# Optimization experiments

Measured on AMD Instinct MI355X. Metric: run time of the kernel, lower is better.

Reference implementation:

```python
import jax, jax.numpy as jnp
import numpy as np
from functools import partial

STRIDES = (8, 16, 32)
SIZES = ((80, 80), (40, 40), (20, 20))
NUM_CLASSES = 80
NMS_THR = 0.65
SCORE_THR = 0.01
MAX_DET = 100  # fixed-size NMS output (padded; validity = scores > 0)


def setup_inputs() -> dict:
    key = jax.random.key(0)
    ks = jax.random.split(key, 9)
    B = 32
    out = {}
    for i, (h, w) in enumerate(SIZES):
        out[f"cls{i}"] = jax.random.normal(ks[3 * i], (B, NUM_CLASSES, h, w), jnp.float32)
        out[f"reg{i}"] = jax.random.normal(ks[3 * i + 1], (B, 4, h, w), jnp.float32)
        out[f"obj{i}"] = jax.random.normal(ks[3 * i + 2], (B, 1, h, w), jnp.float32)
    return out


def _grid_points():
    # MlvlPointGenerator.grid_priors(with_stride=True), offset=0: (x, y, stride, stride)
    pts = []
    for (h, w), s in zip(SIZES, STRIDES):
        xs = jnp.arange(w, dtype=jnp.float32) * s
        ys = jnp.arange(h, dtype=jnp.float32) * s
        xx, yy = jnp.meshgrid(xs, ys)  # [h, w], x varies fastest -> matches NHWC flatten
        st = jnp.full((h * w,), float(s), jnp.float32)
        pts.append(jnp.stack([xx.ravel(), yy.ravel(), st, st], axis=-1))
    return jnp.concatenate(pts, axis=0)  # [A, 4]


def _flatten(t, c):
    # [N, C, H, W] -> [N, H*W, C]  (permute(0,2,3,1).reshape)
    return t.transpose(0, 2, 3, 1).reshape(t.shape[0], -1, c)


def _decode(points, reg):
    # YOLOXBBoxDecoder: center = pred_xy * stride + point, wh = exp(pred_wh) * stride
    stride = points[:, 2:]                       # [A, 2]
    xys = reg[..., :2] * stride + points[:, :2]  # [B, A, 2]
    whs = jnp.exp(reg[..., 2:]) * stride         # [B, A, 2]
    return jnp.concatenate([xys - whs * 0.5, xys + whs * 0.5], axis=-1)  # x1y1x2y2


def _iou_one_vs_all(b, boxes):
    # b: [4], boxes: [A, 4]
    tl = jnp.maximum(b[:2], boxes[:, :2])
    br = jnp.minimum(b[2:], boxes[:, 2:])
    wh = jnp.clip(br - tl, 0.0)
    inter = wh[:, 0] * wh[:, 1]
    a1 = (b[2] - b[0]) * (b[3] - b[1])
    a2 = (boxes[:, 2] - boxes[:, 0]) * (boxes[:, 3] - boxes[:, 1])
    return inter / (a1 + a2 - inter + 1e-6)


def _nms_image(boxes, cls_scores, objectness):
    # boxes [A,4], cls_scores [A,C] (post-sigmoid), objectness [A] (post-sigmoid)
    max_scores = jnp.max(cls_scores, axis=1)
    labels = jnp.argmax(cls_scores, axis=1)
    scores = max_scores * objectness
    live = jnp.where(scores >= SCORE_THR, scores, -jnp.inf)  # score_thr filter

    # batched_nms: offset boxes per class so boxes of different labels never overlap
    offset = jax.lax.stop_gradient(jnp.max(jnp.abs(boxes)) + 1.0)
    boxes_off = jax.lax.stop_gradient(boxes) + labels.astype(boxes.dtype)[:, None] * offset

    def body(i, state):
        live, keep, kscores = state
        best = jnp.argmax(live)
        kscores = kscores.at[i].set(live[best])
        keep = keep.at[i].set(best)
        iou = _iou_one_vs_all(boxes_off[best], boxes_off)
        live = jnp.where(iou > NMS_THR, -jnp.inf, live)
        live = live.at[best].set(-jnp.inf)
        return live, keep, kscores

    keep0 = jnp.zeros((MAX_DET,), jnp.int32)
    ks0 = jnp.full((MAX_DET,), -jnp.inf, boxes.dtype)
    _, keep, kscores = jax.lax.fori_loop(0, MAX_DET, body, (live, keep0, ks0))

    valid = kscores > -jnp.inf
    out_boxes = jnp.where(valid[:, None], boxes[keep], 0.0)
    out_scores = jnp.where(valid, scores[keep], 0.0)
    out_labels = jnp.where(valid, labels[keep], -1)
    return out_boxes, out_scores, out_labels, valid


def _forward(cls0, cls1, cls2, reg0, reg1, reg2, obj0, obj1, obj2):
    B = cls0.shape[0]
    flat_cls = jax.nn.sigmoid(jnp.concatenate([_flatten(c, NUM_CLASSES) for c in (cls0, cls1, cls2)], axis=1))
    flat_reg = jnp.concatenate([_flatten(r, 4) for r in (reg0, reg1, reg2)], axis=1)
    flat_obj = jax.nn.sigmoid(jnp.concatenate([_flatten(o, 1) for o in (obj0, obj1, obj2)], axis=1))[..., 0]
    points = _grid_points()
    boxes = _decode(points, flat_reg)  # [B, A, 4]
    return jax.vmap(_nms_image)(boxes, flat_cls, flat_obj)


@jax.jit
def reference(cls0, cls1, cls2, reg0, reg1, reg2, obj0, obj1, obj2):
    return _forward(cls0, cls1, cls2, reg0, reg1, reg2, obj0, obj1, obj2)
```

## Files before the change

kernel.cpp:

```cpp
#include <hip/hip_runtime.h>
#include <cmath>

typedef unsigned int uint;
typedef unsigned long long ull;

#define BATCH 32
#define NA 8400
#define NC 80
#define MAXDET 100
#define NMSTHR 0.65f
#define SCTHR 0.01f

#define NT 1024
#define NW (NT / 64)
#define EPT 9
#define NBINS 4096
#define CAP 512

#define DGROUPS 132

__device__ __forceinline__ float stable_sigmoid(float x) {
    if (x >= 0.f) return 1.f / (1.f + expf(-x));
    float e = expf(x);
    return e / (1.f + e);
}

template<int HW, int W, int S>
__device__ __forceinline__ void decode_blk(
    const float* __restrict__ cls, const float* __restrict__ reg,
    const float* __restrict__ obj, int b, int p0, int w, int lane, int ag0,
    float (*s_m)[64], int (*s_c)[64],
    float4* __restrict__ wboxes, int* __restrict__ wlabels, uint* __restrict__ wkeys)
{
    int p = p0 + lane;
    bool valid = (p < HW);
    int pc = valid ? p : (HW - 1);

    const float* cbase = cls + (size_t)b * NC * HW + (size_t)(w * 20) * HW + pc;
    float v[20];
    #pragma unroll
    for (int i = 0; i < 20; ++i) v[i] = cbase[(size_t)i * HW];
    float m = v[0]; int c = 0;
    #pragma unroll
    for (int i = 1; i < 20; ++i)
        if (v[i] > m) { m = v[i]; c = i; }

    s_m[w][lane] = m;
    s_c[w][lane] = c + w * 20;
    __syncthreads();

    if (w == 0) {
        float mm = s_m[0][lane]; int cc = s_c[0][lane];
        #pragma unroll
        for (int ww = 1; ww < 4; ++ww) {
            float om = s_m[ww][lane]; int oc = s_c[ww][lane];
            if (om > mm) { mm = om; cc = oc; }
        }
        const float* rb = reg + (size_t)b * 4 * HW + pc;
        float r0 = rb[0];
        float r1 = rb[HW];
        float r2 = rb[2 * (size_t)HW];
        float r3 = rb[3 * (size_t)HW];
        float ov = obj[(size_t)b * HW + pc];

        int y = pc / W;
        int x = pc - y * W;
        float sc = stable_sigmoid(mm) * stable_sigmoid(ov);
        float cx = r0 * (float)S + (float)x * (float)S;
        float cy = r1 * (float)S + (float)y * (float)S;
        float bw = expf(r2) * (float)S;
        float bh = expf(r3) * (float)S;

        if (valid) {
            int ag = ag0 + lane;
            wboxes[ag]  = make_float4(cx - bw * 0.5f, cy - bh * 0.5f,
                                      cx + bw * 0.5f, cy + bh * 0.5f);
            wlabels[ag] = cc;
            wkeys[ag]   = (sc >= SCTHR) ? ~__float_as_uint(sc) : 0xFFFFFFFFu;
        }
    }
}

__global__ __launch_bounds__(256) void decode_kernel(
    const float* __restrict__ cls0, const float* __restrict__ reg0, const float* __restrict__ obj0,
    const float* __restrict__ cls1, const float* __restrict__ reg1, const float* __restrict__ obj1,
    const float* __restrict__ cls2, const float* __restrict__ reg2, const float* __restrict__ obj2,
    float4* __restrict__ wboxes, int* __restrict__ wlabels, uint* __restrict__ wkeys)
{
    __shared__ float s_m[4][64];
    __shared__ int   s_c[4][64];

    int bid  = blockIdx.x;
    int b    = bid / DGROUPS;
    int g    = bid - b * DGROUPS;
    int t    = threadIdx.x;
    int w    = t >> 6;
    int lane = t & 63;

    if (g < 100) {
        int p0 = g * 64;
        decode_blk<6400, 80, 8>(cls0, reg0, obj0, b, p0, w, lane,
                                b * NA + p0, s_m, s_c, wboxes, wlabels, wkeys);
    } else if (g < 125) {
        int p0 = (g - 100) * 64;
        decode_blk<1600, 40, 16>(cls1, reg1, obj1, b, p0, w, lane,
                                 b * NA + 6400 + p0, s_m, s_c, wboxes, wlabels, wkeys);
    } else {
        int p0 = (g - 125) * 64;
        decode_blk<400, 20, 32>(cls2, reg2, obj2, b, p0, w, lane,
                                b * NA + 8000 + p0, s_m, s_c, wboxes, wlabels, wkeys);
    }
}

__global__ __launch_bounds__(NT) void nms_kernel(
    const float4* __restrict__ wboxes, const int* __restrict__ wlabels,
    const uint* __restrict__ wkeys, float* __restrict__ out)
{
    int b = blockIdx.x;
    int t = threadIdx.x;
    int lane = t & 63;
    int wv = t >> 6;
    const float4* boxes  = wboxes  + (size_t)b * NA;
    const int*    labels = wlabels + (size_t)b * NA;
    const uint*   keys   = wkeys   + (size_t)b * NA;

    __shared__ uint   s_hist[NBINS];
    __shared__ uint   s_cum[NBINS + 1];
    __shared__ uint   s_wsum[NW];
    __shared__ ull    s_skey[CAP];
    __shared__ float4 s_cbox[CAP];
    __shared__ float  s_ca[CAP];
    __shared__ int    s_clb[CAP];
    __shared__ float  s_kbox[MAXDET][4];
    __shared__ float  s_ka1[MAXDET];
    __shared__ int    s_kidx[MAXDET];
    __shared__ float  s_kscr[MAXDET];
    __shared__ int    s_klab[MAXDET];
    __shared__ float  s_red[NW];
    __shared__ float  s_off;
    __shared__ int    s_kept, s_winlo, s_winhi, s_nsel;

    float m = 0.f;
    #pragma unroll
    for (int w = 0; w < EPT; ++w) {
        int e = t + w * NT;
        if (e < NA) {
            float4 v = boxes[e];
            m = fmaxf(m, fmaxf(fmaxf(fabsf(v.x), fabsf(v.y)),
                               fmaxf(fabsf(v.z), fabsf(v.w))));
        }
    }
    #pragma unroll
    for (int o = 32; o >= 1; o >>= 1) m = fmaxf(m, __shfl_xor(m, o));
    if (lane == 0) s_red[wv] = m;
    for (int i = t; i < NBINS; i += NT) s_hist[i] = 0;
    if (t == 0) { s_kept = 0; s_winlo = 0; }
    __syncthreads();
    if (t == 0) {
        float mm = 0.f;
        for (int w = 0; w < NW; ++w) mm = fmaxf(mm, s_red[w]);
        s_off = mm + 1.f;
    }
    #pragma unroll
    for (int w = 0; w < EPT; ++w) {
        int e = t + w * NT;
        if (e < NA) {
            uint k = keys[e];
            if (k != 0xFFFFFFFFu) atomicAdd(&s_hist[k >> 20], 1u);
        }
    }
    __syncthreads();
    float off = s_off;

    uint l0 = s_hist[4 * t], l1 = s_hist[4 * t + 1],
         l2 = s_hist[4 * t + 2], l3 = s_hist[4 * t + 3];
    uint L = l0 + l1 + l2 + l3;
    uint ls = L;
    #pragma unroll
    for (int o = 1; o < 64; o <<= 1) {
        uint v = __shfl_up(ls, o);
        if (lane >= o) ls += v;
    }
    if (lane == 63) s_wsum[wv] = ls;
    __syncthreads();
    if (t < NW) {
        uint v = s_wsum[t];
        uint vs = v;
        #pragma unroll
        for (int o = 1; o < NW; o <<= 1) {
            uint u = __shfl_up(vs, o);
            if ((t & 63) >= o) vs += u;
        }
        s_wsum[t] = vs - v;
    }
    __syncthreads();
    uint base = s_wsum[wv] + (ls - L);
    s_cum[4 * t]     = base;
    s_cum[4 * t + 1] = base + l0;
    s_cum[4 * t + 2] = base + l0 + l1;
    s_cum[4 * t + 3] = base + l0 + l1 + l2;
    if (t == NT - 1) s_cum[NBINS] = base + L;

    for (;;) {
        __syncthreads();
        int kept = s_kept, winlo = s_winlo;
        uint remaining = s_cum[NBINS] - s_cum[winlo];
        if (kept >= MAXDET || winlo >= NBINS || remaining == 0u) break;
        if (t == 0) { s_winhi = winlo + 1; s_nsel = 0; }
        if (t < CAP) s_skey[t] = ~0ull;
        __syncthreads();
        uint cl = s_cum[winlo];
        #pragma unroll
        for (int q = 0; q < 4; ++q) {
            int i = t + q * NT;
            if (i >= winlo && i < NBINS) {
                bool p0 = (s_cum[i + 1] - cl) <= (uint)CAP;
                bool p1 = (i + 1 < NBINS) && ((s_cum[i + 2] - cl) <= (uint)CAP);
                if (p0 && !p1) s_winhi = i + 1;
            }
        }
        __syncthreads();
        int winhi = s_winhi;

        #pragma unroll
        for (int w = 0; w < EPT; ++w) {
            int e = t + w * NT;
            bool q = false;
            uint k = 0;
            if (e < NA) {
                k = keys[e];
                if (k != 0xFFFFFFFFu) {
                    int bin = (int)(k >> 20);
                    q = (bin >= winlo && bin < winhi);
                }
            }
            ull mask = __ballot(q);
            if (mask) {
                int leader = __ffsll(mask) - 1;
                int pbase = 0;
                if (lane == leader) pbase = atomicAdd(&s_nsel, __popcll(mask));
                pbase = __shfl(pbase, leader);
                if (q) {
                    int pos = pbase + __popcll(mask & ((1ull << lane) - 1ull));
                    if (pos < CAP) s_skey[pos] = ((ull)k << 32) | (uint)e;
                }
            }
        }
        __syncthreads();
        int nsel = s_nsel; if (nsel > CAP) nsel = CAP;

        ull k = (t < CAP) ? s_skey[t] : ~0ull;
        for (int k2 = 2; k2 <= CAP; k2 <<= 1) {
            for (int j = k2 >> 1; j > 0; j >>= 1) {
                if (j >= 64) {
                    if (t < CAP) s_skey[t] = k;
                    __syncthreads();
                    if (t < CAP) {
                        ull kp = s_skey[t ^ j];
                        bool low = (t & j) == 0;
                        bool up  = (t & k2) == 0;
                        k = ((k < kp) == (low == up)) ? k : kp;
                    }
                    __syncthreads();
                } else if (t < CAP) {
                    ull kp = __shfl_xor(k, j);
                    bool low = (t & j) == 0;
                    bool up  = (t & k2) == 0;
                    k = ((k < kp) == (low == up)) ? k : kp;
                }
            }
        }
        if (t < CAP) s_skey[t] = k;
        __syncthreads();

        if (t < nsel) {
            ull sk = s_skey[t];
            if (sk != ~0ull) {
                int idx = (int)(sk & 0xFFFFFFFFull);
                float4 rb = boxes[idx];
                int lb = labels[idx];
                float lo = (float)lb * off;
                float c0 = rb.x + lo, c1 = rb.y + lo;
                float c2 = rb.z + lo, c3 = rb.w + lo;
                s_cbox[t] = make_float4(c0, c1, c2, c3);
                s_ca[t]   = (c2 - c0) * (c3 - c1);
                s_clb[t]  = lb;
            }
        }
        __syncthreads();

        if (t < 64) {
            int kept2 = s_kept;
            for (int cb = 0; cb < nsel && kept2 < MAXDET; cb += 64) {
                int ci = cb + lane;
                ull sk = (ci < nsel) ? s_skey[ci] : ~0ull;
                bool has = (sk != ~0ull);
                int idx = 0, lab = 0;
                float sc = 0.f, c0 = 0.f, c1 = 0.f, c2 = 0.f, c3 = 0.f, ca = 0.f;
                if (has) {
                    idx = (int)(sk & 0xFFFFFFFFull);
                    sc  = __uint_as_float(~(uint)(sk >> 32));
                    float4 cbx = s_cbox[ci];
                    c0 = cbx.x; c1 = cbx.y; c2 = cbx.z; c3 = cbx.w;
                    ca = s_ca[ci];
                    lab = s_clb[ci];
                    for (int q = 0; q < kept2; ++q) {
                        float tlx = fmaxf(s_kbox[q][0], c0);
                        float tly = fmaxf(s_kbox[q][1], c1);
                        float brx = fminf(s_kbox[q][2], c2);
                        float bry = fminf(s_kbox[q][3], c3);
                        float ww = fmaxf(brx - tlx, 0.f);
                        float hh = fmaxf(bry - tly, 0.f);
                        float inter = ww * hh;
                        float iou = inter / (s_ka1[q] + ca - inter + 1e-6f);
                        if (iou > NMSTHR) { has = false; break; }
                    }
                }
                ull am = __ballot(has);
                while (am && kept2 < MAXDET) {
                    int f = __ffsll(am) - 1;
                    float f0 = __shfl(c0, f), f1 = __shfl(c1, f);
                    float f2 = __shfl(c2, f), f3 = __shfl(c3, f);
                    float fa = __shfl(ca, f);
                    int   fidx = __shfl(idx, f);
                    int   flab = __shfl(lab, f);
                    float fsc  = __shfl(sc, f);
                    if (lane == 0) {
                        s_kbox[kept2][0] = f0; s_kbox[kept2][1] = f1;
                        s_kbox[kept2][2] = f2; s_kbox[kept2][3] = f3;
                        s_ka1[kept2] = fa; s_kidx[kept2] = fidx;
                        s_kscr[kept2] = fsc; s_klab[kept2] = flab;
                    }
                    kept2++;
                    if (lane == f) has = false;
                    if (has) {
                        float tlx = fmaxf(f0, c0), tly = fmaxf(f1, c1);
                        float brx = fminf(f2, c2), bry = fminf(f3, c3);
                        float ww = fmaxf(brx - tlx, 0.f), hh = fmaxf(bry - tly, 0.f);
                        float inter = ww * hh;
                        float iou = inter / (fa + ca - inter + 1e-6f);
                        if (iou > NMSTHR) has = false;
                    }
                    am = __ballot(has);
                }
            }
            if (lane == 0) s_kept = kept2;
        }
        __syncthreads();
        if (t == 0) s_winlo = s_winhi;
    }
    __syncthreads();

    if (t < MAXDET) {
        int kept = s_kept;
        float4 obx = make_float4(0.f, 0.f, 0.f, 0.f);
        float osc = 0.f, olab = -1.f, oval = 0.f;
        if (t < kept) {
            int idx = s_kidx[t];
            obx  = boxes[idx];
            osc  = s_kscr[t];
            olab = (float)s_klab[t];
            oval = 1.f;
        }
        float* ob = out + ((size_t)b * MAXDET + t) * 4;
        ob[0] = obx.x; ob[1] = obx.y; ob[2] = obx.z; ob[3] = obx.w;
        out[BATCH * MAXDET * 4 + b * MAXDET + t] = osc;
        out[BATCH * MAXDET * 5 + b * MAXDET + t] = olab;
        out[BATCH * MAXDET * 6 + b * MAXDET + t] = oval;
    }
}

extern "C" void kernel_launch(void* const* d_in, const int* in_sizes, int n_in,
                              void* d_out, int out_size, void* d_ws, size_t ws_size,
                              hipStream_t stream) {
    const float* cls0 = (const float*)d_in[0];
    const float* reg0 = (const float*)d_in[1];
    const float* obj0 = (const float*)d_in[2];
    const float* cls1 = (const float*)d_in[3];
    const float* reg1 = (const float*)d_in[4];
    const float* obj1 = (const float*)d_in[5];
    const float* cls2 = (const float*)d_in[6];
    const float* reg2 = (const float*)d_in[7];
    const float* obj2 = (const float*)d_in[8];

    char* ws = (char*)d_ws;
    size_t nBA = (size_t)BATCH * NA;
    float4* wboxes  = (float4*)ws;
    int*    wlabels = (int*)(ws + nBA * 16);
    uint*   wkeys   = (uint*)(ws + nBA * 20);

    decode_kernel<<<BATCH * DGROUPS, 256, 0, stream>>>(
        cls0, reg0, obj0, cls1, reg1, obj1, cls2, reg2, obj2,
        wboxes, wlabels, wkeys);

    nms_kernel<<<BATCH, NT, 0, stream>>>(wboxes, wlabels, wkeys, (float*)d_out);
}
```

Baseline: 166.4 us.

## Precompute intra-chunk suppression bitmask and fuse histogram into max-reduction pass

Within each 64-candidate chunk, every lane now computes its IoU against all earlier candidates up front and packs the results into a suppression bitmask. The serial greedy loop then only does a ballot plus a bit test per kept box, replacing eight shuffles and an IoU per step. The histogram atomics are also merged into the same pass over the boxes as the max-abs reduction, which removes one loop over global memory and one barrier. The cost is a full 64-way IoU loop per chunk even when few candidates survive.

```diff
diff --git a/kernel.cpp b/kernel.cpp
--- a/kernel.cpp
+++ b/kernel.cpp
@@ -140,6 +140,9 @@
     __shared__ float  s_off;
     __shared__ int    s_kept, s_winlo, s_winhi, s_nsel;
 
+    for (int i = t; i < NBINS; i += NT) s_hist[i] = 0;
+    if (t == 0) { s_kept = 0; s_winlo = 0; }
+    __syncthreads();
     float m = 0.f;
     #pragma unroll
     for (int w = 0; w < EPT; ++w) {
@@ -148,29 +151,19 @@
             float4 v = boxes[e];
             m = fmaxf(m, fmaxf(fmaxf(fabsf(v.x), fabsf(v.y)),
                                fmaxf(fabsf(v.z), fabsf(v.w))));
+            uint k = keys[e];
+            if (k != 0xFFFFFFFFu) atomicAdd(&s_hist[k >> 20], 1u);
         }
     }
     #pragma unroll
     for (int o = 32; o >= 1; o >>= 1) m = fmaxf(m, __shfl_xor(m, o));
     if (lane == 0) s_red[wv] = m;
-    for (int i = t; i < NBINS; i += NT) s_hist[i] = 0;
-    if (t == 0) { s_kept = 0; s_winlo = 0; }
     __syncthreads();
     if (t == 0) {
         float mm = 0.f;
         for (int w = 0; w < NW; ++w) mm = fmaxf(mm, s_red[w]);
         s_off = mm + 1.f;
     }
-    #pragma unroll
-    for (int w = 0; w < EPT; ++w) {
-        int e = t + w * NT;
-        if (e < NA) {
-            uint k = keys[e];
-            if (k != 0xFFFFFFFFu) atomicAdd(&s_hist[k >> 20], 1u);
-        }
-    }
-    __syncthreads();
-    float off = s_off;
 
     uint l0 = s_hist[4 * t], l1 = s_hist[4 * t + 1],
          l2 = s_hist[4 * t + 2], l3 = s_hist[4 * t + 3];
@@ -200,6 +193,7 @@
     s_cum[4 * t + 2] = base + l0 + l1;
     s_cum[4 * t + 3] = base + l0 + l1 + l2;
     if (t == NT - 1) s_cum[NBINS] = base + L;
+    float off;
 
     for (;;) {
         __syncthreads();
@@ -273,6 +267,7 @@
         if (t < CAP) s_skey[t] = k;
         __syncthreads();
 
+        off = s_off;
         if (t < nsel) {
             ull sk = s_skey[t];
             if (sk != ~0ull) {
@@ -294,10 +289,10 @@
             for (int cb = 0; cb < nsel && kept2 < MAXDET; cb += 64) {
                 int ci = cb + lane;
                 ull sk = (ci < nsel) ? s_skey[ci] : ~0ull;
-                bool has = (sk != ~0ull);
+                bool alive = (sk != ~0ull);
                 int idx = 0, lab = 0;
                 float sc = 0.f, c0 = 0.f, c1 = 0.f, c2 = 0.f, c3 = 0.f, ca = 0.f;
-                if (has) {
+                if (alive) {
                     idx = (int)(sk & 0xFFFFFFFFull);
                     sc  = __uint_as_float(~(uint)(sk >> 32));
                     float4 cbx = s_cbox[ci];
@@ -313,35 +308,34 @@
                         float hh = fmaxf(bry - tly, 0.f);
                         float inter = ww * hh;
                         float iou = inter / (s_ka1[q] + ca - inter + 1e-6f);
-                        if (iou > NMSTHR) { has = false; break; }
+                        if (iou > NMSTHR) { alive = false; break; }
                     }
                 }
-                ull am = __ballot(has);
-                while (am && kept2 < MAXDET) {
+                ull supmask = 0ull;
+                int lim = nsel - cb; if (lim > 64) lim = 64;
+                for (int i = 0; i < lim; ++i) {
+                    float4 bi = s_cbox[cb + i];
+                    float  ai = s_ca[cb + i];
+                    float tlx = fmaxf(bi.x, c0), tly = fmaxf(bi.y, c1);
+                    float brx = fminf(bi.z, c2), bry = fminf(bi.w, c3);
+                    float ww = fmaxf(brx - tlx, 0.f), hh = fmaxf(bry - tly, 0.f);
+                    float inter = ww * hh;
+                    float iou = inter / (ai + ca - inter + 1e-6f);
+                    if (i < lane && iou > NMSTHR) supmask |= (1ull << i);
+                }
+                ull am = __ballot(alive);
+                while (am != 0ull && kept2 < MAXDET) {
                     int f = __ffsll(am) - 1;
-                    float f0 = __shfl(c0, f), f1 = __shfl(c1, f);
-                    float f2 = __shfl(c2, f), f3 = __shfl(c3, f);
-                    float fa = __shfl(ca, f);
-                    int   fidx = __shfl(idx, f);
-                    int   flab = __shfl(lab, f);
-                    float fsc  = __shfl(sc, f);
-                    if (lane == 0) {
-                        s_kbox[kept2][0] = f0; s_kbox[kept2][1] = f1;
-                        s_kbox[kept2][2] = f2; s_kbox[kept2][3] = f3;
-                        s_ka1[kept2] = fa; s_kidx[kept2] = fidx;
-                        s_kscr[kept2] = fsc; s_klab[kept2] = flab;
+                    if (lane == f) {
+                        s_kbox[kept2][0] = c0; s_kbox[kept2][1] = c1;
+                        s_kbox[kept2][2] = c2; s_kbox[kept2][3] = c3;
+                        s_ka1[kept2] = ca; s_kidx[kept2] = idx;
+                        s_kscr[kept2] = sc; s_klab[kept2] = lab;
+                        alive = false;
                     }
                     kept2++;
-                    if (lane == f) has = false;
-                    if (has) {
-                        float tlx = fmaxf(f0, c0), tly = fmaxf(f1, c1);
-                        float brx = fminf(f2, c2), bry = fminf(f3, c3);
-                        float ww = fmaxf(brx - tlx, 0.f), hh = fmaxf(bry - tly, 0.f);
-                        float inter = ww * hh;
-                        float iou = inter / (fa + ca - inter + 1e-6f);
-                        if (iou > NMSTHR) has = false;
-                    }
-                    am = __ballot(has);
+                    if (alive && ((supmask >> f) & 1ull)) alive = false;
+                    am = __ballot(alive);
                 }
             }
             if (lane == 0) s_kept = kept2;
```

Result: slower. 171.0 us (+2.8%).
